# Optimization experiments

Measured on AMD Instinct MI355X. Metric: run time of the kernel, lower is better.

Reference implementation:

```python
import jax, jax.numpy as jnp
import numpy as np

B, T, C, H = 4, 2048, 1024, 16
HS = C // H  # 64
THRESH_INIT = (5 + 1) / 12 * 0.01  # (layer_idx+1)/n_layer * final_token_threshold


def _layernorm(x, w, b, eps=1e-5):
    mu = jnp.mean(x, axis=-1, keepdims=True)
    var = jnp.var(x, axis=-1, keepdims=True)
    return (x - mu) * jax.lax.rsqrt(var + eps) * w + b


def setup_inputs() -> dict:
    key = jax.random.key(0)
    ks = jax.random.split(key, 8)
    s = 0.02
    inp = {
        'x': jax.random.normal(ks[0], (B, T, C), dtype=jnp.float32),
        'attention_mask': jnp.ones((B, T), dtype=jnp.float32),
        'protected_mask': jnp.zeros((B, T), dtype=jnp.float32),
        'ln1_w': jnp.ones((C,), jnp.float32),
        'ln1_b': jnp.zeros((C,), jnp.float32),
        'c_attn_w': jax.random.normal(ks[1], (3 * C, C), jnp.float32) * s,
        'c_attn_b': jnp.zeros((3 * C,), jnp.float32),
        'c_proj_w': jax.random.normal(ks[2], (C, C), jnp.float32) * s,
        'c_proj_b': jnp.zeros((C,), jnp.float32),
        'ln2_w': jnp.ones((C,), jnp.float32),
        'ln2_b': jnp.zeros((C,), jnp.float32),
        'fc_w': jax.random.normal(ks[3], (4 * C, C), jnp.float32) * s,
        'fc_b': jnp.zeros((4 * C,), jnp.float32),
        'fcproj_w': jax.random.normal(ks[4], (C, 4 * C), jnp.float32) * s,
        'fcproj_b': jnp.zeros((C,), jnp.float32),
        'threshold': jnp.asarray(THRESH_INIT, jnp.float32),
    }
    return inp


def reference(x, attention_mask, protected_mask, ln1_w, ln1_b, c_attn_w, c_attn_b,
              c_proj_w, c_proj_b, ln2_w, ln2_b, fc_w, fc_b, fcproj_w, fcproj_b, threshold):
    b, t, c = x.shape
    # --- attention with importance scores ---
    h = _layernorm(x, ln1_w, ln1_b)
    qkv = h @ c_attn_w.T + c_attn_b                      # (B,T,3C)
    q, k, v = jnp.split(qkv, 3, axis=-1)
    q = q.reshape(b, t, H, HS).transpose(0, 2, 1, 3)     # (B,H,T,hs)
    k = k.reshape(b, t, H, HS).transpose(0, 2, 1, 3)
    v = v.reshape(b, t, H, HS).transpose(0, 2, 1, 3)
    att = jnp.einsum('bhqd,bhkd->bhqk', q, k) / np.sqrt(HS)
    causal = jnp.tril(jnp.ones((t, t), dtype=bool))      # (T,T)
    att = jnp.where(causal[None, None], att, -jnp.inf)
    att = jnp.where(attention_mask[:, None, None, :] != 0, att, -jnp.inf)
    att = jax.nn.softmax(att, axis=-1)                   # (B,H,T,T)
    y = jnp.einsum('bhqk,bhkd->bhqd', att, v)
    y = y.transpose(0, 2, 1, 3).reshape(b, t, c)
    y = y @ c_proj_w.T + c_proj_b
    importance = att.mean(axis=1).mean(axis=1)           # (B,T): mean over heads, then queries
    # --- pruning ---
    x = x + y
    pruning_mask = (importance >= threshold).astype(x.dtype)  # hard mode
    pruning_mask = jnp.where(protected_mask > 0, jnp.ones_like(pruning_mask), pruning_mask)
    combined_mask = attention_mask * pruning_mask
    x = x * combined_mask[..., None]
    # --- MLP ---
    m = _layernorm(x, ln2_w, ln2_b)
    m = jax.nn.gelu(m @ fc_w.T + fc_b, approximate=False)
    x = x + (m @ fcproj_w.T + fcproj_b)
    pruning_loss = jnp.asarray(0.0, x.dtype)  # hard mode / lambda=0
    return (x, combined_mask, pruning_loss)
```

## Files before the change

### kernel.cpp

```cpp
#include <hip/hip_runtime.h>
#include <math.h>

#define B_ 4
#define T_ 2048
#define C_ 1024
#define H_ 16
#define NROWS (B_*T_)

typedef short s8v  __attribute__((ext_vector_type(8)));
typedef float f4v  __attribute__((ext_vector_type(4)));
typedef unsigned short u16v4 __attribute__((ext_vector_type(4)));

#define QSCALE 0.1803368801111f

static __device__ __forceinline__ unsigned short f2bf(float x) {
    unsigned u = __float_as_uint(x);
    unsigned r = u + 0x7fffu + ((u >> 16) & 1u);
    return (unsigned short)(r >> 16);
}

static __device__ __forceinline__ float fexp2(float x) {
    return __builtin_amdgcn_exp2f(x);
}

static __device__ __forceinline__ void gload_lds16(const void* g, void* l) {
    __builtin_amdgcn_global_load_lds(
        (const __attribute__((address_space(1))) void*)g,
        (__attribute__((address_space(3))) void*)l, 16, 0, 0);
}

__global__ __launch_bounds__(256) void prep_kernel(
        const float* __restrict__ x, const float* __restrict__ w,
        const float* __restrict__ b, unsigned short* __restrict__ out,
        const float* __restrict__ wsrc, unsigned short* __restrict__ wdst,
        float* __restrict__ imp, int* __restrict__ nsurv)
{
    int row = blockIdx.x;
    int tid = threadIdx.x;
    int widx = row * 96 + tid;
    if (tid < 96) {
        float4 v = ((const float4*)wsrc)[widx];
        u16v4 o = { f2bf(v.x), f2bf(v.y), f2bf(v.z), f2bf(v.w) };
        *(u16v4*)(wdst + (size_t)widx*4) = o;
    }
    if (row < 32) imp[row*256 + tid] = 0.f;
    if (row == 32 && tid < 8) nsurv[tid] = 0;

    const float4* xr = (const float4*)(x + (size_t)row * C_);
    float4 v = xr[tid];
    float s  = v.x + v.y + v.z + v.w;
    float ss = v.x*v.x + v.y*v.y + v.z*v.z + v.w*v.w;
    #pragma unroll
    for (int off = 32; off > 0; off >>= 1) {
        s  += __shfl_down(s,  off, 64);
        ss += __shfl_down(ss, off, 64);
    }
    __shared__ float rs[4], rss[4];
    __shared__ float smu, srstd;
    int wave = tid >> 6, lane = tid & 63;
    if (lane == 0) { rs[wave] = s; rss[wave] = ss; }
    __syncthreads();
    if (tid == 0) {
        float S  = rs[0]+rs[1]+rs[2]+rs[3];
        float SS = rss[0]+rss[1]+rss[2]+rss[3];
        float mu = S * (1.0f/C_);
        float var = SS * (1.0f/C_) - mu*mu;
        smu = mu; srstd = rsqrtf(var + 1e-5f);
    }
    __syncthreads();
    float mu = smu, rstd = srstd;
    float4 wv = ((const float4*)w)[tid];
    float4 bv = ((const float4*)b)[tid];
    u16v4 o;
    o.x = f2bf((v.x-mu)*rstd*wv.x + bv.x);
    o.y = f2bf((v.y-mu)*rstd*wv.y + bv.y);
    o.z = f2bf((v.z-mu)*rstd*wv.z + bv.z);
    o.w = f2bf((v.w-mu)*rstd*wv.w + bv.w);
    *(u16v4*)(out + (size_t)row * C_ + tid*4) = o;
}

__global__ __launch_bounds__(256) void ln_bf16(const float* __restrict__ x,
        const float* __restrict__ w, const float* __restrict__ b,
        unsigned short* __restrict__ out, const int* __restrict__ flag, int nrows)
{
    if (flag && flag[0] == 0) return;
    int tid = threadIdx.x;
    __shared__ float rs[4], rss[4];
    __shared__ float smu, srstd;
    int wave = tid >> 6, lane = tid & 63;
    for (int row = blockIdx.x; row < nrows; row += gridDim.x) {
        const float4* xr = (const float4*)(x + (size_t)row * C_);
        float4 v = xr[tid];
        float s  = v.x + v.y + v.z + v.w;
        float ss = v.x*v.x + v.y*v.y + v.z*v.z + v.w*v.w;
        #pragma unroll
        for (int off = 32; off > 0; off >>= 1) {
            s  += __shfl_down(s,  off, 64);
            ss += __shfl_down(ss, off, 64);
        }
        if (lane == 0) { rs[wave] = s; rss[wave] = ss; }
        __syncthreads();
        if (tid == 0) {
            float S  = rs[0]+rs[1]+rs[2]+rs[3];
            float SS = rss[0]+rss[1]+rss[2]+rss[3];
            float mu = S * (1.0f/C_);
            float var = SS * (1.0f/C_) - mu*mu;
            smu = mu; srstd = rsqrtf(var + 1e-5f);
        }
        __syncthreads();
        float mu = smu, rstd = srstd;
        float4 wv = ((const float4*)w)[tid];
        float4 bv = ((const float4*)b)[tid];
        u16v4 o;
        o.x = f2bf((v.x-mu)*rstd*wv.x + bv.x);
        o.y = f2bf((v.y-mu)*rstd*wv.y + bv.y);
        o.z = f2bf((v.z-mu)*rstd*wv.z + bv.z);
        o.w = f2bf((v.w-mu)*rstd*wv.w + bv.w);
        *(u16v4*)(out + (size_t)row * C_ + tid*4) = o;
        __syncthreads();
    }
}

__global__ __launch_bounds__(256) void cvt3_bf16(
        const float* __restrict__ cprojw, const float* __restrict__ fcw,
        const float* __restrict__ fcpw,
        unsigned short* __restrict__ wproj, unsigned short* __restrict__ wfc,
        unsigned short* __restrict__ wfcp, const int* __restrict__ flag)
{
    if (flag[0] == 0) return;
    const int total = 9*C_*C_/4;
    const int n1 = C_*C_/4;
    const int n2 = n1 + C_*C_;
    for (int i = blockIdx.x * 256 + threadIdx.x; i < total; i += gridDim.x * 256) {
        const float* src; unsigned short* dst; int j;
        if (i < n1)      { src = cprojw; dst = wproj; j = i; }
        else if (i < n2) { src = fcw;    dst = wfc;   j = i - n1; }
        else             { src = fcpw;   dst = wfcp;  j = i - n2; }
        float4 v = ((const float4*)src)[j];
        u16v4 o = { f2bf(v.x), f2bf(v.y), f2bf(v.z), f2bf(v.w) };
        *(u16v4*)(dst + (size_t)j*4) = o;
    }
}

#define STG(gbase_, ldsarr_, ah_, kt_, bb_) do { \
    gload_lds16(gbase_ + (size_t)((ah_)*128)*1024 + (kt_)*64, \
                &ldsarr_[bb_][(((ah_)*128) + (w<<3))*64]); \
    gload_lds16(gbase_ + (size_t)((ah_)*128 + 64)*1024 + (kt_)*64, \
                &ldsarr_[bb_][(((ah_)*128 + 64) + (w<<3))*64]); \
} while (0)

#define PHASE(ah_, bh_, ...) do { \
    s8v af[4][2], bf[2][2]; \
    _Pragma("unroll") \
    for (int i2 = 0; i2 < 4; i2++) { \
        int arow = ((ah_)*128 + wr*64 + i2*16 + l16)*64; \
        af[i2][0] = *(const s8v*)&As[bb][arow + (((quad)     ^ (l16&7))<<3)]; \
        af[i2][1] = *(const s8v*)&As[bb][arow + (((4 + quad) ^ (l16&7))<<3)]; \
    } \
    _Pragma("unroll") \
    for (int j2 = 0; j2 < 2; j2++) { \
        int brow = ((bh_)*128 + wc*32 + j2*16 + l16)*64; \
        bf[j2][0] = *(const s8v*)&Bs[bb][brow + (((quad)     ^ (l16&7))<<3)]; \
        bf[j2][1] = *(const s8v*)&Bs[bb][brow + (((4 + quad) ^ (l16&7))<<3)]; \
    } \
    __VA_ARGS__; \
    asm volatile("s_barrier" ::: "memory"); \
    asm volatile("s_waitcnt lgkmcnt(0)" ::: "memory"); \
    __builtin_amdgcn_sched_barrier(0); \
    __builtin_amdgcn_s_setprio(1); \
    _Pragma("unroll") \
    for (int i2 = 0; i2 < 4; i2++) \
        _Pragma("unroll") \
        for (int j2 = 0; j2 < 2; j2++) { \
            acc[(ah_)*4+i2][(bh_)*2+j2] = __builtin_amdgcn_mfma_f32_16x16x32_bf16( \
                af[i2][0], bf[j2][0], acc[(ah_)*4+i2][(bh_)*2+j2], 0, 0, 0); \
            acc[(ah_)*4+i2][(bh_)*2+j2] = __builtin_amdgcn_mfma_f32_16x16x32_bf16( \
                af[i2][1], bf[j2][1], acc[(ah_)*4+i2][(bh_)*2+j2], 0, 0, 0); \
        } \
    __builtin_amdgcn_s_setprio(0); \
    __builtin_amdgcn_sched_barrier(0); \
    asm volatile("s_barrier" ::: "memory"); \
} while (0)

__global__ __launch_bounds__(512, 2) void gemm_qk_8ph(
    const unsigned short* __restrict__ A,
    const unsigned short* __restrict__ Bw,
    const float* __restrict__ bias,
    unsigned short* __restrict__ qh, unsigned short* __restrict__ kh)
{
    __shared__ unsigned short As[2][256*64];
    __shared__ unsigned short Bs[2][256*64];

    const int tid  = threadIdx.x;
    const int w    = tid >> 6, lane = tid & 63;
// ... 7 lines not shown
    const int m0  = (vb >> 3) << 8;
    const int n0  = (vb & 7) << 8;

    const unsigned short* gA0 = A  + (size_t)(m0 + rl) * 1024 + kc * 8;
    const unsigned short* gB0 = Bw + (size_t)(n0 + rl) * 1024 + kc * 8;

    STG(gA0, As, 0, 0, 0);
    STG(gB0, Bs, 1, 0, 0);
    STG(gA0, As, 1, 0, 0);
    STG(gB0, Bs, 0, 0, 0);
    STG(gA0, As, 0, 1, 1);
    STG(gB0, Bs, 1, 1, 1);

    f4v acc[8][4];
    #pragma unroll
    for (int i = 0; i < 8; i++)
        #pragma unroll
        for (int j = 0; j < 4; j++) {
            acc[i][j][0] = 0.f; acc[i][j][1] = 0.f;
            acc[i][j][2] = 0.f; acc[i][j][3] = 0.f;
        }

    #pragma unroll 2
    for (int t = 0; t < 16; ++t) {
        const int bb = t & 1, nb = bb ^ 1;
        if (t < 15) asm volatile("s_waitcnt vmcnt(4)" ::: "memory");
        else        asm volatile("s_waitcnt vmcnt(0)" ::: "memory");
        asm volatile("s_barrier" ::: "memory");
        __builtin_amdgcn_sched_barrier(0);
        PHASE(0, 0, if (t < 15) STG(gA0, As, 1, t+1, nb));
        PHASE(0, 1, if (t < 15) STG(gB0, Bs, 0, t+1, nb));
        PHASE(1, 1, if (t < 14) STG(gA0, As, 0, t+2, bb));
        PHASE(1, 0, if (t < 14) STG(gB0, Bs, 1, t+2, bb));
    }

    #pragma unroll
    for (int j = 0; j < 4; j++) {
        int ncol = n0 + ((j >> 1) << 7) + (wc << 5) + ((j & 1) << 4) + l16;
        float bv = bias[ncol];
        int sec = ncol >> 10;
        int hh = (ncol & 1023) >> 6, dd = ncol & 63;
        unsigned short* basep = (sec == 0) ? qh : kh;
        bool qsec = (sec == 0);
        #pragma unroll
        for (int i = 0; i < 8; i++) {
            int mbase = m0 + ((i >> 2) << 7) + (wr << 6) + ((i & 3) << 4) + (quad << 2);
            #pragma unroll
            for (int reg = 0; reg < 4; reg++) {
                int m = mbase + reg;
                float v = acc[i][j][reg] + bv;
                if (qsec) v *= QSCALE;
                int b_ = m >> 11, tt = m & 2047;
                basep[(((size_t)(b_*H_ + hh))*T_ + tt)*64 + dd] = f2bf(v);
            }
        }
    }
}

template<int EPI>
__global__ __launch_bounds__(256) void gemm_bf16(
    const unsigned short* __restrict__ A,
    const unsigned short* __restrict__ Bw,
    const float* __restrict__ bias,
    const float* __restrict__ res,
    float* __restrict__ Cout, unsigned short* __restrict__ Cbf,
    int K, int lda, int ldb, int ldc, int ncoff,
    const float* __restrict__ cmv,
    unsigned short* __restrict__ qh, unsigned short* __restrict__ kh,
    unsigned short* __restrict__ vh, const int* __restrict__ flag,
    int nbx, int nby)
{
    if (flag && flag[0] == 0) return;
    __shared__ unsigned short As[128*64];
    __shared__ unsigned short Bs[128*64];
    int tid = threadIdx.x;
    int w = tid >> 6, lane = tid & 63, quad = lane >> 4, l16 = lane & 15;
    int wr = w >> 1, wc = w & 1;

    int nvb = nbx * nby;
    int vb0 = blockIdx.y * gridDim.x + blockIdx.x;
    int vstride = gridDim.x * gridDim.y;

    for (int vb = vb0; vb < nvb; vb += vstride) {
        int n0 = (vb % nbx) * 128;
        int m0 = (vb / nbx) * 128;

        size_t offA[4], offB[4];
        #pragma unroll
        for (int j = 0; j < 4; j++) {
            int ci = j*256 + tid;
            int mr = ci >> 3, kcs = ci & 7;
            int kc = kcs ^ (mr & 7);
            offA[j] = (size_t)(m0 + mr) * lda + kc*8;
            offB[j] = (size_t)(n0 + mr) * ldb + kc*8;
        }

        f4v acc[4][4];
        #pragma unroll
        for (int i = 0; i < 4; i++)
            #pragma unroll
            for (int j = 0; j < 4; j++) { acc[i][j][0]=0.f; acc[i][j][1]=0.f; acc[i][j][2]=0.f; acc[i][j][3]=0.f; }

        for (int k0 = 0; k0 < K; k0 += 64) {
            __syncthreads();
            #pragma unroll
            for (int j = 0; j < 4; j++) {
                gload_lds16(A  + offA[j] + k0, &As[(j*256 + (w<<6))*8]);
                gload_lds16(Bw + offB[j] + k0, &Bs[(j*256 + (w<<6))*8]);
            }
            __syncthreads();
            #pragma unroll
            for (int c = 0; c < 2; c++) {
                s8v af[4], bf[4];
                int sw = ((c<<2) + quad) ^ (l16 & 7);
                #pragma unroll
                for (int i = 0; i < 4; i++) {
                    int mr = wr*64 + i*16 + l16;
                    af[i] = *(const s8v*)&As[mr*64 + sw*8];
                    int nr = wc*64 + i*16 + l16;
                    bf[i] = *(const s8v*)&Bs[nr*64 + sw*8];
                }
                #pragma unroll
                for (int i = 0; i < 4; i++)
                    #pragma unroll
                    for (int j = 0; j < 4; j++)
                        acc[i][j] = __builtin_amdgcn_mfma_f32_16x16x32_bf16(af[i], bf[j], acc[i][j], 0, 0, 0);
            }
        }

        #pragma unroll
        for (int j = 0; j < 4; j++) {
            int ncol = n0 + wc*64 + j*16 + l16;
            float bv = bias ? bias[ncol] : 0.f;
            int hh = 0, dd = 0;
            bool qsec = false;
            unsigned short* basep = nullptr;
            if (EPI == 3) {
                int ncolg = ncol + ncoff;
                int sec = ncolg >> 10;
                int hn = ncolg & 1023;
                hh = hn >> 6; dd = hn & 63;
                basep = (sec == 0) ? qh : (sec == 1) ? kh : vh;
                qsec = (sec == 0);
            }
            #pragma unroll
            for (int i = 0; i < 4; i++) {
                #pragma unroll
                for (int reg = 0; reg < 4; reg++) {
                    int m = m0 + wr*64 + i*16 + quad*4 + reg;
                    float v = acc[i][j][reg] + bv;
                    if (EPI == 1) {
                        v = 0.5f * v * (1.0f + erff(v * 0.70710678118654752f));
                        Cbf[(size_t)m*ldc + ncol] = f2bf(v);
                    } else if (EPI == 2) {
                        Cout[(size_t)m*ldc + ncol] = v + res[(size_t)m*ldc + ncol];
                    } else if (EPI == 3) {
                        if (qsec) v *= QSCALE;
                        int bb = m >> 11, t = m & 2047;
                        basep[(((size_t)(bb*H_ + hh))*T_ + t)*64 + dd] = f2bf(v);
                    } else if (EPI == 4) {
                        Cout[(size_t)m*ldc + ncol] = (res[(size_t)m*ldc + ncol] + v) * cmv[m];
                    }
                }
            }
        }
    }
}

#define RS_LOADK(K_, it_) do { \
    int k0_ = (it_) * 64; \
    _Pragma("unroll") \
    for (int c_ = 0; c_ < 2; c_++) \
        _Pragma("unroll") \
        for (int nt_ = 0; nt_ < 4; nt_++) \
            K_[c_][nt_] = *(const s8v*)(kp + (size_t)(k0_ + nt_*16 + l16)*64 + c_*32 + quad*8); \
} while (0)

#define RS_COMP(K_, it_) do { \
    int k0_ = (it_) * 64; \
    float mk[4]; \
    _Pragma("unroll") \
    for (int nt_ = 0; nt_ < 4; nt_++) mk[nt_] = msk01[k0_ + nt_*16 + l16]; \
    bool allm = __all(mk[0] != 0.f && mk[1] != 0.f && mk[2] != 0.f && mk[3] != 0.f); \
    _Pragma("unroll") \
    for (int qf = 0; qf < 4; qf++) { \
        f4v acc[4]; \
        _Pragma("unroll") \
        for (int nt_ = 0; nt_ < 4; nt_++) { acc[nt_][0]=0.f; acc[nt_][1]=0.f; acc[nt_][2]=0.f; acc[nt_][3]=0.f; } \
        _Pragma("unroll") \
        for (int c_ = 0; c_ < 2; c_++) \
            _Pragma("unroll") \
            for (int nt_ = 0; nt_ < 4; nt_++) \
                acc[nt_] = __builtin_amdgcn_mfma_f32_16x16x32_bf16(aQ[qf][c_], K_[c_][nt_], acc[nt_], 0, 0, 0); \
        if ((it_) < qt && allm) { \
            _Pragma("unroll") \
            for (int nt_ = 0; nt_ < 4; nt_++) \
                _Pragma("unroll") \
                for (int reg = 0; reg < 4; reg++) \
                    lrow[qf][reg] += fexp2(acc[nt_][reg]); \
        } else if ((it_) < qt) { \
            _Pragma("unroll") \
            for (int nt_ = 0; nt_ < 4; nt_++) \
                _Pragma("unroll") \
                for (int reg = 0; reg < 4; reg++) \
                    lrow[qf][reg] += fexp2(acc[nt_][reg]) * mk[nt_]; \
        } else { \
            _Pragma("unroll") \
            for (int nt_ = 0; nt_ < 4; nt_++) { \
                int kg = k0_ + nt_*16 + l16; \
                _Pragma("unroll") \
                for (int reg = 0; reg < 4; reg++) { \
                    float me = (kg <= q0 + qf*16 + quad*4 + reg) ? mk[nt_] : 0.f; \
                    lrow[qf][reg] += fexp2(acc[nt_][reg]) * me; \
                } \
            } \
        } \
// ... 183 lines not shown
                int qt2 = qtn + 4;
                if (qt2 < 32) {
                    CS_LOADQT(AQa, LVa, qt2);
                    CS_COMPQT(AQb, LVb, qtn);
                    qt = qt2;
                    continue;
                } else {
                    CS_COMPQT(AQb, LVb, qtn);
                    break;
                }
            } else {
                CS_COMPQT(AQa, LVa, qt);
                break;
            }
        }
    }

    #pragma unroll
    for (int nt = 0; nt < 4; nt++) {
        float v = cs[nt] * mk[nt];
        v += __shfl_xor(v, 16);
        v += __shfl_xor(v, 32);
        if (quad == 0) cred[w][nt*16 + l16] = v;
    }
    __syncthreads();
    if (tid < 64)
        atomicAdd(&imp[b*T_ + k0 + tid],
                  cred[0][tid] + cred[1][tid] + cred[2][tid] + cred[3][tid]);
}

__global__ __launch_bounds__(256) void mask_finalize(
    const float* __restrict__ imp, const float* __restrict__ amask,
    const float* __restrict__ prot, const float* __restrict__ thr,
    float* __restrict__ mask_out, float* __restrict__ loss_out,
    int* __restrict__ nsurv)
{
    int i = blockIdx.x * 256 + threadIdx.x;
    float impv = imp[i] * (1.0f / (float)(H_ * T_));
    float pm = (impv >= thr[0]) ? 1.f : 0.f;
    if (prot[i] > 0.f) pm = 1.f;
    float cm = amask[i] * pm;
    mask_out[i] = cm;
    if (i == 0) loss_out[0] = 0.f;
    unsigned long long bal = __ballot(cm != 0.f);
    int cnt = __popcll(bal);
    __shared__ int bs;
    if (threadIdx.x == 0) bs = 0;
    __syncthreads();
    if ((threadIdx.x & 63) == 0 && cnt) atomicAdd(&bs, cnt);
    __syncthreads();
    if (threadIdx.x == 0 && bs) atomicAdd(nsurv, bs);
}

__global__ __launch_bounds__(256) void attn_full(
    const unsigned short* __restrict__ qh, const unsigned short* __restrict__ kh,
    const unsigned short* __restrict__ vh, const float* __restrict__ amask,
    unsigned short* __restrict__ y, const int* __restrict__ flag)
{
    if (flag[0] == 0) return;
    __shared__ unsigned short Ks[64][72];
    __shared__ unsigned short Vt[64][72];
    __shared__ unsigned short Ps[4][16][72];
    __shared__ float mks[64];

    int tid = threadIdx.x;
    int w = tid >> 6, lane = tid & 63, quad = lane >> 4, l16 = lane & 15;
    int nqt = T_ / 64;

    for (int vb = blockIdx.x; vb < B_*H_*nqt; vb += gridDim.x) {
        int qt = vb % nqt;
        int bh = vb / nqt;
        int b = bh >> 4, h = bh & 15;
        int q0 = qt * 64;

        const unsigned short* qp = qh + (size_t)bh * T_ * 64;
        const unsigned short* kp = kh + (size_t)bh * T_ * 64;
        const unsigned short* vp = vh + (size_t)bh * T_ * 64;

        int qrow = q0 + 16*w + l16;
        s8v aQ0 = *(const s8v*)(qp + (size_t)qrow*64 + quad*8);
        s8v aQ1 = *(const s8v*)(qp + (size_t)qrow*64 + 32 + quad*8);

        int qwmax = q0 + 16*w + 15;
        int ntiles = qt + 1;
        int qg = q0 + 16*w + quad*4;

        float lrow[4] = {0.f, 0.f, 0.f, 0.f};
        for (int it = 0; it < ntiles; ++it) {
            int k0 = it * 64;
            __syncthreads();
            for (int cid = tid; cid < 512; cid += 256) {
                int row = cid >> 3, ch = cid & 7;
                *(s8v*)&Ks[row][ch*8] = *(const s8v*)(kp + (size_t)(k0+row)*64 + ch*8);
            }
            if (tid < 64) mks[tid] = amask[b*T_ + k0 + tid];
            __syncthreads();
            if (k0 > qwmax) continue;
            f4v accS[4];
            #pragma unroll
            for (int nt = 0; nt < 4; nt++) { accS[nt][0]=0.f; accS[nt][1]=0.f; accS[nt][2]=0.f; accS[nt][3]=0.f; }
            #pragma unroll
            for (int nt = 0; nt < 4; nt++) {
                s8v b0 = *(const s8v*)&Ks[nt*16 + l16][quad*8];
                s8v b1 = *(const s8v*)&Ks[nt*16 + l16][32 + quad*8];
                accS[nt] = __builtin_amdgcn_mfma_f32_16x16x32_bf16(aQ0, b0, accS[nt], 0, 0, 0);
                accS[nt] = __builtin_amdgcn_mfma_f32_16x16x32_bf16(aQ1, b1, accS[nt], 0, 0, 0);
            }
            #pragma unroll
            for (int nt = 0; nt < 4; nt++) {
                int kg = k0 + nt*16 + l16;
                float mkv = mks[nt*16 + l16];
                #pragma unroll
                for (int reg = 0; reg < 4; reg++) {
                    bool val = (kg <= qg + reg) && (mkv != 0.f);
                    float e = fexp2(accS[nt][reg]);
                    lrow[reg] += val ? e : 0.f;
                }
            }
        }
        float linv[4];
        #pragma unroll
        for (int reg = 0; reg < 4; reg++) {
            float v = lrow[reg];
            v += __shfl_xor(v, 1); v += __shfl_xor(v, 2);
            v += __shfl_xor(v, 4); v += __shfl_xor(v, 8);
            linv[reg] = (v > 0.f) ? 1.0f / v : 0.f;
        }

        f4v accO[4];
        #pragma unroll
        for (int nt = 0; nt < 4; nt++) { accO[nt][0]=0.f; accO[nt][1]=0.f; accO[nt][2]=0.f; accO[nt][3]=0.f; }

        for (int it = 0; it < ntiles; ++it) {
            int k0 = it * 64;
            __syncthreads();
            for (int cid = tid; cid < 512; cid += 256) {
                int row = cid >> 3, ch = cid & 7;
                s8v kv = *(const s8v*)(kp + (size_t)(k0+row)*64 + ch*8);
                *(s8v*)&Ks[row][ch*8] = kv;
                s8v vv = *(const s8v*)(vp + (size_t)(k0+row)*64 + ch*8);
                #pragma unroll
                for (int j = 0; j < 8; j++) Vt[ch*8 + j][row] = (unsigned short)vv[j];
            }
            if (tid < 64) mks[tid] = amask[b*T_ + k0 + tid];
            __syncthreads();
            if (k0 > qwmax) continue;
            f4v accS[4];
            #pragma unroll
            for (int nt = 0; nt < 4; nt++) { accS[nt][0]=0.f; accS[nt][1]=0.f; accS[nt][2]=0.f; accS[nt][3]=0.f; }
            #pragma unroll
            for (int nt = 0; nt < 4; nt++) {
                s8v b0 = *(const s8v*)&Ks[nt*16 + l16][quad*8];
                s8v b1 = *(const s8v*)&Ks[nt*16 + l16][32 + quad*8];
                accS[nt] = __builtin_amdgcn_mfma_f32_16x16x32_bf16(aQ0, b0, accS[nt], 0, 0, 0);
                accS[nt] = __builtin_amdgcn_mfma_f32_16x16x32_bf16(aQ1, b1, accS[nt], 0, 0, 0);
            }
            #pragma unroll
            for (int nt = 0; nt < 4; nt++) {
                int kg = k0 + nt*16 + l16;
                float mkv = mks[nt*16 + l16];
                #pragma unroll
                for (int reg = 0; reg < 4; reg++) {
                    bool val = (kg <= qg + reg) && (mkv != 0.f);
                    float p = val ? fexp2(accS[nt][reg]) * linv[reg] : 0.f;
                    Ps[w][quad*4 + reg][nt*16 + l16] = f2bf(p);
                }
            }
            s8v aP0 = *(const s8v*)&Ps[w][l16][quad*8];
            s8v aP1 = *(const s8v*)&Ps[w][l16][32 + quad*8];
            #pragma unroll
            for (int nt = 0; nt < 4; nt++) {
                s8v bv0 = *(const s8v*)&Vt[nt*16 + l16][quad*8];
                s8v bv1 = *(const s8v*)&Vt[nt*16 + l16][32 + quad*8];
                accO[nt] = __builtin_amdgcn_mfma_f32_16x16x32_bf16(aP0, bv0, accO[nt], 0, 0, 0);
                accO[nt] = __builtin_amdgcn_mfma_f32_16x16x32_bf16(aP1, bv1, accO[nt], 0, 0, 0);
            }
        }
        #pragma unroll
        for (int nt = 0; nt < 4; nt++) {
            #pragma unroll
            for (int reg = 0; reg < 4; reg++) {
                int q = q0 + 16*w + quad*4 + reg;
                y[((size_t)(b*T_ + q))*C_ + h*64 + nt*16 + l16] = f2bf(accO[nt][reg]);
            }
        }
        __syncthreads();
    }
}

__global__ __launch_bounds__(256) void ap_fc(const int* __restrict__ nsurv,
        const float* __restrict__ ln2b, const float* __restrict__ fcw,
        const float* __restrict__ fcb, float* __restrict__ abuf)
{
    if (nsurv[0] != 0) return;
    int j = blockIdx.x * 4 + (threadIdx.x >> 6);
    int lane = threadIdx.x & 63;
    const float4* wr = (const float4*)(fcw + (size_t)j * C_);
    const float4* bb = (const float4*)ln2b;
    float s = 0.f;
    #pragma unroll
    for (int k = 0; k < 4; k++) {
        float4 a = bb[lane + 64*k];
        float4 wv = wr[lane + 64*k];
        s += a.x*wv.x + a.y*wv.y + a.z*wv.z + a.w*wv.w;
    }
    #pragma unroll
    for (int off = 32; off > 0; off >>= 1) s += __shfl_down(s, off, 64);
    if (lane == 0) {
        float v = fcb[j] + s;
        abuf[j] = 0.5f * v * (1.0f + erff(v * 0.70710678118654752f));
    }
}

__global__ __launch_bounds__(256) void ap_fcp(const int* __restrict__ nsurv,
        const float* __restrict__ abuf, const float* __restrict__ fcpw,
        const float* __restrict__ fcpb, float* __restrict__ rowbuf)
{
    if (nsurv[0] != 0) return;
    int c = blockIdx.x * 4 + (threadIdx.x >> 6);
    int lane = threadIdx.x & 63;
    const float4* wr = (const float4*)(fcpw + (size_t)c * (4*C_));
    const float4* ab = (const float4*)abuf;
    float s = 0.f;
    #pragma unroll
    for (int k = 0; k < 16; k++) {
        float4 a = ab[lane + 64*k];
        float4 wv = wr[lane + 64*k];
        s += a.x*wv.x + a.y*wv.y + a.z*wv.z + a.w*wv.w;
    }
    #pragma unroll
    for (int off = 32; off > 0; off >>= 1) s += __shfl_down(s, off, 64);
    if (lane == 0) rowbuf[c] = fcpb[c] + s;
}

__global__ __launch_bounds__(256) void ap_bcast(const int* __restrict__ nsurv,
        const float* __restrict__ rowbuf, float* __restrict__ out_x)
{
    if (nsurv[0] != 0) return;
    float4 v = ((const float4*)rowbuf)[threadIdx.x];
    for (int r = blockIdx.x; r < NROWS; r += gridDim.x)
        ((float4*)(out_x + (size_t)r * C_))[threadIdx.x] = v;
}

extern "C" void kernel_launch(void* const* d_in, const int* in_sizes, int n_in,
                              void* d_out, int out_size, void* d_ws, size_t ws_size,
                              hipStream_t stream) {
    const float* x       = (const float*)d_in[0];
    const float* amask   = (const float*)d_in[1];
    const float* prot    = (const float*)d_in[2];
    const float* ln1w    = (const float*)d_in[3];
    const float* ln1b    = (const float*)d_in[4];
    const float* cattn_w = (const float*)d_in[5];
    const float* cattn_b = (const float*)d_in[6];
    const float* cproj_w = (const float*)d_in[7];
    const float* cproj_b = (const float*)d_in[8];
    const float* ln2w    = (const float*)d_in[9];
    const float* ln2b    = (const float*)d_in[10];
    const float* fcw     = (const float*)d_in[11];
    const float* fcb     = (const float*)d_in[12];
    const float* fcpw    = (const float*)d_in[13];
    const float* fcpb    = (const float*)d_in[14];
    const float* thr     = (const float*)d_in[15];

    unsigned short* wqkv  = (unsigned short*)d_ws;
    unsigned short* wproj = wqkv  + (size_t)3*C_*C_;
    unsigned short* wfc   = wproj + (size_t)C_*C_;
    unsigned short* wfcp  = wfc   + (size_t)4*C_*C_;
    unsigned short* hbuf  = wfcp  + (size_t)4*C_*C_;
    unsigned short* qh    = hbuf  + (size_t)NROWS*C_;
    unsigned short* kh    = qh    + (size_t)NROWS*C_;
    unsigned short* vh    = kh    + (size_t)NROWS*C_;
    unsigned short* cbuf  = qh;
    float* imp    = (float*)(vh + (size_t)NROWS*C_);
    int*   nsurv  = (int*)(imp + NROWS);
    float* abuf   = (float*)(nsurv + 8);
    float* rowbuf = abuf + 4*C_;
    float* linvbuf = rowbuf + C_;

    float* out_x    = (float*)d_out;
    float* out_mask = out_x + (size_t)NROWS*C_;
    float* out_loss = out_mask + NROWS;

    hipLaunchKernelGGL(prep_kernel, dim3(NROWS), dim3(256), 0, stream,
                       x, ln1w, ln1b, hbuf, cattn_w, wqkv, imp, nsurv);
    hipLaunchKernelGGL(gemm_qk_8ph, dim3(256), dim3(512), 0, stream,
                       hbuf, wqkv, cattn_b, qh, kh);
    hipLaunchKernelGGL(attn_rowsum, dim3(64*32), dim3(256), 0, stream,
                       qh, kh, amask, linvbuf);
    hipLaunchKernelGGL(attn_colsum, dim3(64*32), dim3(256), 0, stream,
                       qh, kh, amask, linvbuf, imp);
    hipLaunchKernelGGL(mask_finalize, dim3(NROWS/256), dim3(256), 0, stream,
                       imp, amask, prot, thr, out_mask, out_loss, nsurv);

    hipLaunchKernelGGL(cvt3_bf16, dim3(512), dim3(256), 0, stream,
                       cproj_w, fcw, fcpw, wproj, wfc, wfcp, nsurv);
    hipLaunchKernelGGL((gemm_bf16<3>), dim3(512), dim3(256), 0, stream,
                       hbuf, wqkv + (size_t)2048*C_, cattn_b + 2048, nullptr, nullptr, nullptr,
                       C_, C_, C_, 0, 2048, nullptr, qh, kh, vh, nsurv, 8, 64);
    hipLaunchKernelGGL(attn_full, dim3(512), dim3(256), 0, stream,
                       qh, kh, vh, amask, hbuf, nsurv);
    hipLaunchKernelGGL((gemm_bf16<4>), dim3(512), dim3(256), 0, stream,
                       hbuf, wproj, cproj_b, x, out_x, nullptr,
                       C_, C_, C_, C_, 0, out_mask, nullptr, nullptr, nullptr, nsurv, 8, 64);
    hipLaunchKernelGGL(ln_bf16, dim3(512), dim3(256), 0, stream,
                       out_x, ln2w, ln2b, hbuf, nsurv, NROWS);
    for (int j = 0; j < 2; j++) {
        hipLaunchKernelGGL((gemm_bf16<1>), dim3(512), dim3(256), 0, stream,
                           hbuf, wfc + (size_t)j*2048*C_, fcb + j*2048, nullptr, nullptr, cbuf,
                           C_, C_, C_, 2048, 0, nullptr, nullptr, nullptr, nullptr, nsurv, 16, 64);
        hipLaunchKernelGGL((gemm_bf16<2>), dim3(512), dim3(256), 0, stream,
                           cbuf, wfcp + (size_t)j*2048, (j == 0) ? fcpb : nullptr, out_x, out_x, nullptr,
                           2048, 2048, 4*C_, C_, 0, nullptr, nullptr, nullptr, nullptr, nsurv, 8, 64);
    }

    hipLaunchKernelGGL(ap_fc,    dim3(4*C_/4), dim3(256), 0, stream, nsurv, ln2b, fcw, fcb, abuf);
    hipLaunchKernelGGL(ap_fcp,   dim3(C_/4),   dim3(256), 0, stream, nsurv, abuf, fcpw, fcpb, rowbuf);
    hipLaunchKernelGGL(ap_bcast, dim3(512),    dim3(256), 0, stream, nsurv, rowbuf, out_x);
}
```

Baseline: 306.1 us.

## Merge post-mask launches into one persistent kernel with grid barriers

Replaces the chain of conditional tail launches (weight conversion, V projection, attention, projections, layernorm, MLP GEMMs and the all-pruned shortcut kernels) with a single persistent kernel. Phases are separated by a software grid barrier built on atomic counters. This is meant to remove per-launch overhead and the cost of many early-return launches. The risk is deadlock if not all blocks are co-resident, and the fixed 256-block grid may reduce parallelism in the dense path.

```diff
diff --git a/kernel.cpp b/kernel.cpp
--- a/kernel.cpp
+++ b/kernel.cpp
@@ -27,6 +27,25 @@
     __builtin_amdgcn_global_load_lds(
         (const __attribute__((address_space(1))) void*)g,
         (__attribute__((address_space(3))) void*)l, 16, 0, 0);
+}
+
+static __device__ __forceinline__ void gsync(int* bar, int nblk) {
+    __syncthreads();
+    __threadfence();
+    if (threadIdx.x == 0) {
+        int* cnt = bar;
+        int* gen = bar + 1;
+        int g = __hip_atomic_load(gen, __ATOMIC_ACQUIRE, __HIP_MEMORY_SCOPE_AGENT);
+        int a = __hip_atomic_fetch_add(cnt, 1, __ATOMIC_ACQ_REL, __HIP_MEMORY_SCOPE_AGENT);
+        if (a == nblk - 1) {
+            __hip_atomic_store(cnt, 0, __ATOMIC_RELAXED, __HIP_MEMORY_SCOPE_AGENT);
+            __hip_atomic_fetch_add(gen, 1, __ATOMIC_ACQ_REL, __HIP_MEMORY_SCOPE_AGENT);
+        } else {
+            while (__hip_atomic_load(gen, __ATOMIC_ACQUIRE, __HIP_MEMORY_SCOPE_AGENT) == g)
+                __builtin_amdgcn_s_sleep(2);
+        }
+    }
+    __syncthreads();
 }
 
 __global__ __launch_bounds__(256) void prep_kernel(
@@ -77,69 +96,6 @@
     o.z = f2bf((v.z-mu)*rstd*wv.z + bv.z);
     o.w = f2bf((v.w-mu)*rstd*wv.w + bv.w);
     *(u16v4*)(out + (size_t)row * C_ + tid*4) = o;
-}
-
-__global__ __launch_bounds__(256) void ln_bf16(const float* __restrict__ x,
-        const float* __restrict__ w, const float* __restrict__ b,
-        unsigned short* __restrict__ out, const int* __restrict__ flag, int nrows)
-{
-    if (flag && flag[0] == 0) return;
-    int tid = threadIdx.x;
-    __shared__ float rs[4], rss[4];
-    __shared__ float smu, srstd;
-    int wave = tid >> 6, lane = tid & 63;
-    for (int row = blockIdx.x; row < nrows; row += gridDim.x) {
-        const float4* xr = (const float4*)(x + (size_t)row * C_);
-        float4 v = xr[tid];
-        float s  = v.x + v.y + v.z + v.w;
-        float ss = v.x*v.x + v.y*v.y + v.z*v.z + v.w*v.w;
-        #pragma unroll
-        for (int off = 32; off > 0; off >>= 1) {
-            s  += __shfl_down(s,  off, 64);
-            ss += __shfl_down(ss, off, 64);
-        }
-        if (lane == 0) { rs[wave] = s; rss[wave] = ss; }
-        __syncthreads();
-        if (tid == 0) {
-            float S  = rs[0]+rs[1]+rs[2]+rs[3];
-            float SS = rss[0]+rss[1]+rss[2]+rss[3];
-            float mu = S * (1.0f/C_);
-            float var = SS * (1.0f/C_) - mu*mu;
-            smu = mu; srstd = rsqrtf(var + 1e-5f);
-        }
-        __syncthreads();
-        float mu = smu, rstd = srstd;
-        float4 wv = ((const float4*)w)[tid];
-        float4 bv = ((const float4*)b)[tid];
-        u16v4 o;
-        o.x = f2bf((v.x-mu)*rstd*wv.x + bv.x);
-        o.y = f2bf((v.y-mu)*rstd*wv.y + bv.y);
-        o.z = f2bf((v.z-mu)*rstd*wv.z + bv.z);
-        o.w = f2bf((v.w-mu)*rstd*wv.w + bv.w);
-        *(u16v4*)(out + (size_t)row * C_ + tid*4) = o;
-        __syncthreads();
-    }
-}
-
-__global__ __launch_bounds__(256) void cvt3_bf16(
-        const float* __restrict__ cprojw, const float* __restrict__ fcw,
-        const float* __restrict__ fcpw,
-        unsigned short* __restrict__ wproj, unsigned short* __restrict__ wfc,
-        unsigned short* __restrict__ wfcp, const int* __restrict__ flag)
-{
-    if (flag[0] == 0) return;
-    const int total = 9*C_*C_/4;
-    const int n1 = C_*C_/4;
-    const int n2 = n1 + C_*C_;
-    for (int i = blockIdx.x * 256 + threadIdx.x; i < total; i += gridDim.x * 256) {
-        const float* src; unsigned short* dst; int j;
-        if (i < n1)      { src = cprojw; dst = wproj; j = i; }
-        else if (i < n2) { src = fcw;    dst = wfc;   j = i - n1; }
-        else             { src = fcpw;   dst = wfcp;  j = i - n2; }
-        float4 v = ((const float4*)src)[j];
-        u16v4 o = { f2bf(v.x), f2bf(v.y), f2bf(v.z), f2bf(v.w) };
-        *(u16v4*)(dst + (size_t)j*4) = o;
-    }
 }
 
 #define STG(gbase_, ldsarr_, ah_, kt_, bb_) do { \
@@ -253,116 +209,6 @@
                 if (qsec) v *= QSCALE;
                 int b_ = m >> 11, tt = m & 2047;
                 basep[(((size_t)(b_*H_ + hh))*T_ + tt)*64 + dd] = f2bf(v);
-            }
-        }
-    }
-}
-
-template<int EPI>
-__global__ __launch_bounds__(256) void gemm_bf16(
-    const unsigned short* __restrict__ A,
-    const unsigned short* __restrict__ Bw,
-    const float* __restrict__ bias,
-    const float* __restrict__ res,
-    float* __restrict__ Cout, unsigned short* __restrict__ Cbf,
-    int K, int lda, int ldb, int ldc, int ncoff,
-    const float* __restrict__ cmv,
-    unsigned short* __restrict__ qh, unsigned short* __restrict__ kh,
-    unsigned short* __restrict__ vh, const int* __restrict__ flag,
-    int nbx, int nby)
-{
-    if (flag && flag[0] == 0) return;
-    __shared__ unsigned short As[128*64];
-    __shared__ unsigned short Bs[128*64];
-    int tid = threadIdx.x;
-    int w = tid >> 6, lane = tid & 63, quad = lane >> 4, l16 = lane & 15;
-    int wr = w >> 1, wc = w & 1;
-
-    int nvb = nbx * nby;
-    int vb0 = blockIdx.y * gridDim.x + blockIdx.x;
-    int vstride = gridDim.x * gridDim.y;
-
-    for (int vb = vb0; vb < nvb; vb += vstride) {
-        int n0 = (vb % nbx) * 128;
-        int m0 = (vb / nbx) * 128;
-
-        size_t offA[4], offB[4];
-        #pragma unroll
-        for (int j = 0; j < 4; j++) {
-            int ci = j*256 + tid;
-            int mr = ci >> 3, kcs = ci & 7;
-            int kc = kcs ^ (mr & 7);
-            offA[j] = (size_t)(m0 + mr) * lda + kc*8;
-            offB[j] = (size_t)(n0 + mr) * ldb + kc*8;
-        }
-
-        f4v acc[4][4];
-        #pragma unroll
-        for (int i = 0; i < 4; i++)
-            #pragma unroll
-            for (int j = 0; j < 4; j++) { acc[i][j][0]=0.f; acc[i][j][1]=0.f; acc[i][j][2]=0.f; acc[i][j][3]=0.f; }
-
-        for (int k0 = 0; k0 < K; k0 += 64) {
-            __syncthreads();
-            #pragma unroll
-            for (int j = 0; j < 4; j++) {
-                gload_lds16(A  + offA[j] + k0, &As[(j*256 + (w<<6))*8]);
-                gload_lds16(Bw + offB[j] + k0, &Bs[(j*256 + (w<<6))*8]);
-            }
-            __syncthreads();
-            #pragma unroll
-            for (int c = 0; c < 2; c++) {
-                s8v af[4], bf[4];
-                int sw = ((c<<2) + quad) ^ (l16 & 7);
-                #pragma unroll
-                for (int i = 0; i < 4; i++) {
-                    int mr = wr*64 + i*16 + l16;
-                    af[i] = *(const s8v*)&As[mr*64 + sw*8];
-                    int nr = wc*64 + i*16 + l16;
-                    bf[i] = *(const s8v*)&Bs[nr*64 + sw*8];
-                }
-                #pragma unroll
-                for (int i = 0; i < 4; i++)
-                    #pragma unroll
-                    for (int j = 0; j < 4; j++)
-                        acc[i][j] = __builtin_amdgcn_mfma_f32_16x16x32_bf16(af[i], bf[j], acc[i][j], 0, 0, 0);
-            }
-        }
-
-        #pragma unroll
-        for (int j = 0; j < 4; j++) {
-            int ncol = n0 + wc*64 + j*16 + l16;
-            float bv = bias ? bias[ncol] : 0.f;
-            int hh = 0, dd = 0;
-            bool qsec = false;
-            unsigned short* basep = nullptr;
-            if (EPI == 3) {
-                int ncolg = ncol + ncoff;
-                int sec = ncolg >> 10;
-                int hn = ncolg & 1023;
-                hh = hn >> 6; dd = hn & 63;
-                basep = (sec == 0) ? qh : (sec == 1) ? kh : vh;
-                qsec = (sec == 0);
-            }
-            #pragma unroll
-            for (int i = 0; i < 4; i++) {
-                #pragma unroll
-                for (int reg = 0; reg < 4; reg++) {
-                    int m = m0 + wr*64 + i*16 + quad*4 + reg;
-                    float v = acc[i][j][reg] + bv;
-                    if (EPI == 1) {
-                        v = 0.5f * v * (1.0f + erff(v * 0.70710678118654752f));
-                        Cbf[(size_t)m*ldc + ncol] = f2bf(v);
-                    } else if (EPI == 2) {
-                        Cout[(size_t)m*ldc + ncol] = v + res[(size_t)m*ldc + ncol];
-                    } else if (EPI == 3) {
-                        if (qsec) v *= QSCALE;
-                        int bb = m >> 11, t = m & 2047;
-                        basep[(((size_t)(bb*H_ + hh))*T_ + t)*64 + dd] = f2bf(v);
-                    } else if (EPI == 4) {
-                        Cout[(size_t)m*ldc + ncol] = (res[(size_t)m*ldc + ncol] + v) * cmv[m];
-                    }
-                }
             }
         }
     }
@@ -652,16 +498,145 @@
     if (threadIdx.x == 0 && bs) atomicAdd(nsurv, bs);
 }
 
-__global__ __launch_bounds__(256) void attn_full(
+
+static __device__ void cvt3_body(
+        const float* __restrict__ cprojw, const float* __restrict__ fcw,
+        const float* __restrict__ fcpw,
+        unsigned short* __restrict__ wproj, unsigned short* __restrict__ wfc,
+        unsigned short* __restrict__ wfcp)
+{
+    const int total = 9*C_*C_/4;
+    const int n1 = C_*C_/4;
+    const int n2 = n1 + C_*C_;
+    for (int i = blockIdx.x * 256 + threadIdx.x; i < total; i += gridDim.x * 256) {
+        const float* src; unsigned short* dst; int j;
+        if (i < n1)      { src = cprojw; dst = wproj; j = i; }
+        else if (i < n2) { src = fcw;    dst = wfc;   j = i - n1; }
+        else             { src = fcpw;   dst = wfcp;  j = i - n2; }
+        float4 v = ((const float4*)src)[j];
+        u16v4 o = { f2bf(v.x), f2bf(v.y), f2bf(v.z), f2bf(v.w) };
+        *(u16v4*)(dst + (size_t)j*4) = o;
+    }
+}
+
+template<int EPI>
+static __device__ void gemm_body(
+    unsigned short* As, unsigned short* Bs,
+    const unsigned short* __restrict__ A,
+    const unsigned short* __restrict__ Bw,
+    const float* __restrict__ bias,
+    const float* __restrict__ res,
+    float* __restrict__ Cout, unsigned short* __restrict__ Cbf,
+    int K, int lda, int ldb, int ldc, int ncoff,
+    const float* __restrict__ cmv,
+    unsigned short* __restrict__ qh, unsigned short* __restrict__ kh,
+    unsigned short* __restrict__ vh,
+    int nbx, int nby)
+{
+    int tid = threadIdx.x;
+    int w = tid >> 6, lane = tid & 63, quad = lane >> 4, l16 = lane & 15;
+    int wr = w >> 1, wc = w & 1;
+
+    int nvb = nbx * nby;
+    int vb0 = blockIdx.x;
+    int vstride = gridDim.x;
+
+    for (int vb = vb0; vb < nvb; vb += vstride) {
+        int n0 = (vb % nbx) * 128;
+        int m0 = (vb / nbx) * 128;
+
+        size_t offA[4], offB[4];
+        #pragma unroll
+        for (int j = 0; j < 4; j++) {
+            int ci = j*256 + tid;
+            int mr = ci >> 3, kcs = ci & 7;
+            int kc = kcs ^ (mr & 7);
+            offA[j] = (size_t)(m0 + mr) * lda + kc*8;
+            offB[j] = (size_t)(n0 + mr) * ldb + kc*8;
+        }
+
+        f4v acc[4][4];
+        #pragma unroll
+        for (int i = 0; i < 4; i++)
+            #pragma unroll
+            for (int j = 0; j < 4; j++) { acc[i][j][0]=0.f; acc[i][j][1]=0.f; acc[i][j][2]=0.f; acc[i][j][3]=0.f; }
+
+        for (int k0 = 0; k0 < K; k0 += 64) {
+            __syncthreads();
+            #pragma unroll
+            for (int j = 0; j < 4; j++) {
+                gload_lds16(A  + offA[j] + k0, &As[(j*256 + (w<<6))*8]);
+                gload_lds16(Bw + offB[j] + k0, &Bs[(j*256 + (w<<6))*8]);
+            }
+            __syncthreads();
+            #pragma unroll
+            for (int c = 0; c < 2; c++) {
+                s8v af[4], bf[4];
+                int sw = ((c<<2) + quad) ^ (l16 & 7);
+                #pragma unroll
+                for (int i = 0; i < 4; i++) {
+                    int mr = wr*64 + i*16 + l16;
+                    af[i] = *(const s8v*)&As[mr*64 + sw*8];
+                    int nr = wc*64 + i*16 + l16;
+                    bf[i] = *(const s8v*)&Bs[nr*64 + sw*8];
+                }
+                #pragma unroll
+                for (int i = 0; i < 4; i++)
+                    #pragma unroll
+                    for (int j = 0; j < 4; j++)
+                        acc[i][j] = __builtin_amdgcn_mfma_f32_16x16x32_bf16(af[i], bf[j], acc[i][j], 0, 0, 0);
+            }
+        }
+
+        #pragma unroll
+        for (int j = 0; j < 4; j++) {
+            int ncol = n0 + wc*64 + j*16 + l16;
+            float bv = bias ? bias[ncol] : 0.f;
+            int hh = 0, dd = 0;
+            bool qsec = false;
+            unsigned short* basep = nullptr;
+            if (EPI == 3) {
+                int ncolg = ncol + ncoff;
+                int sec = ncolg >> 10;
+                int hn = ncolg & 1023;
+                hh = hn >> 6; dd = hn & 63;
+                basep = (sec == 0) ? qh : (sec == 1) ? kh : vh;
+                qsec = (sec == 0);
+            }
+            #pragma unroll
+            for (int i = 0; i < 4; i++) {
+                #pragma unroll
+                for (int reg = 0; reg < 4; reg++) {
+                    int m = m0 + wr*64 + i*16 + quad*4 + reg;
+                    float v = acc[i][j][reg] + bv;
+                    if (EPI == 1) {
+                        v = 0.5f * v * (1.0f + erff(v * 0.70710678118654752f));
+                        Cbf[(size_t)m*ldc + ncol] = f2bf(v);
+                    } else if (EPI == 2) {
+                        Cout[(size_t)m*ldc + ncol] = v + res[(size_t)m*ldc + ncol];
+                    } else if (EPI == 3) {
+                        if (qsec) v *= QSCALE;
+                        int bb = m >> 11, t = m & 2047;
+                        basep[(((size_t)(bb*H_ + hh))*T_ + t)*64 + dd] = f2bf(v);
+                    } else if (EPI == 4) {
+                        Cout[(size_t)m*ldc + ncol] = (res[(size_t)m*ldc + ncol] + v) * cmv[m];
+                    }
+                }
+            }
+        }
+        __syncthreads();
+    }
+}
+
+static __device__ void attn_full_body(unsigned short* sm,
     const unsigned short* __restrict__ qh, const unsigned short* __restrict__ kh,
     const unsigned short* __restrict__ vh, const float* __restrict__ amask,
-    unsigned short* __restrict__ y, const int* __restrict__ flag)
+    unsigned short* __restrict__ y)
 {
-    if (flag[0] == 0) return;
-    __shared__ unsigned short Ks[64][72];
-    __shared__ unsigned short Vt[64][72];
-    __shared__ unsigned short Ps[4][16][72];
-    __shared__ float mks[64];
+    unsigned short* Ks = sm;
+    unsigned short* Vt = sm + 64*72;
+    unsigned short* Ps = sm + 2*64*72;
+    float* mks = (float*)(sm + 2*64*72 + 4*16*72);
 
     int tid = threadIdx.x;
     int w = tid >> 6, lane = tid & 63, quad = lane >> 4, l16 = lane & 15;
@@ -691,7 +666,7 @@
             __syncthreads();
             for (int cid = tid; cid < 512; cid += 256) {
                 int row = cid >> 3, ch = cid & 7;
-                *(s8v*)&Ks[row][ch*8] = *(const s8v*)(kp + (size_t)(k0+row)*64 + ch*8);
+                *(s8v*)&Ks[row*72 + ch*8] = *(const s8v*)(kp + (size_t)(k0+row)*64 + ch*8);
             }
             if (tid < 64) mks[tid] = amask[b*T_ + k0 + tid];
             __syncthreads();
@@ -701,8 +676,8 @@
             for (int nt = 0; nt < 4; nt++) { accS[nt][0]=0.f; accS[nt][1]=0.f; accS[nt][2]=0.f; accS[nt][3]=0.f; }
             #pragma unroll
             for (int nt = 0; nt < 4; nt++) {
-                s8v b0 = *(const s8v*)&Ks[nt*16 + l16][quad*8];
-                s8v b1 = *(const s8v*)&Ks[nt*16 + l16][32 + quad*8];
+                s8v b0 = *(const s8v*)&Ks[(nt*16 + l16)*72 + quad*8];
+                s8v b1 = *(const s8v*)&Ks[(nt*16 + l16)*72 + 32 + quad*8];
                 accS[nt] = __builtin_amdgcn_mfma_f32_16x16x32_bf16(aQ0, b0, accS[nt], 0, 0, 0);
                 accS[nt] = __builtin_amdgcn_mfma_f32_16x16x32_bf16(aQ1, b1, accS[nt], 0, 0, 0);
             }
@@ -737,10 +712,10 @@
             for (int cid = tid; cid < 512; cid += 256) {
                 int row = cid >> 3, ch = cid & 7;
                 s8v kv = *(const s8v*)(kp + (size_t)(k0+row)*64 + ch*8);
-                *(s8v*)&Ks[row][ch*8] = kv;
+                *(s8v*)&Ks[row*72 + ch*8] = kv;
                 s8v vv = *(const s8v*)(vp + (size_t)(k0+row)*64 + ch*8);
                 #pragma unroll
-                for (int j = 0; j < 8; j++) Vt[ch*8 + j][row] = (unsigned short)vv[j];
+                for (int j = 0; j < 8; j++) Vt[(ch*8 + j)*72 + row] = (unsigned short)vv[j];
             }
             if (tid < 64) mks[tid] = amask[b*T_ + k0 + tid];
             __syncthreads();
@@ -750,8 +725,8 @@
             for (int nt = 0; nt < 4; nt++) { accS[nt][0]=0.f; accS[nt][1]=0.f; accS[nt][2]=0.f; accS[nt][3]=0.f; }
             #pragma unroll
             for (int nt = 0; nt < 4; nt++) {
-                s8v b0 = *(const s8v*)&Ks[nt*16 + l16][quad*8];
-                s8v b1 = *(const s8v*)&Ks[nt*16 + l16][32 + quad*8];
+                s8v b0 = *(const s8v*)&Ks[(nt*16 + l16)*72 + quad*8];
+                s8v b1 = *(const s8v*)&Ks[(nt*16 + l16)*72 + 32 + quad*8];
                 accS[nt] = __builtin_amdgcn_mfma_f32_16x16x32_bf16(aQ0, b0, accS[nt], 0, 0, 0);
                 accS[nt] = __builtin_amdgcn_mfma_f32_16x16x32_bf16(aQ1, b1, accS[nt], 0, 0, 0);
             }
@@ -763,15 +738,15 @@
                 for (int reg = 0; reg < 4; reg++) {
                     bool val = (kg <= qg + reg) && (mkv != 0.f);
                     float p = val ? fexp2(accS[nt][reg]) * linv[reg] : 0.f;
-                    Ps[w][quad*4 + reg][nt*16 + l16] = f2bf(p);
+                    Ps[(w*16 + quad*4 + reg)*72 + nt*16 + l16] = f2bf(p);
                 }
             }
-            s8v aP0 = *(const s8v*)&Ps[w][l16][quad*8];
-            s8v aP1 = *(const s8v*)&Ps[w][l16][32 + quad*8];
+            s8v aP0 = *(const s8v*)&Ps[(w*16 + l16)*72 + quad*8];
+            s8v aP1 = *(const s8v*)&Ps[(w*16 + l16)*72 + 32 + quad*8];
             #pragma unroll
             for (int nt = 0; nt < 4; nt++) {
-                s8v bv0 = *(const s8v*)&Vt[nt*16 + l16][quad*8];
-                s8v bv1 = *(const s8v*)&Vt[nt*16 + l16][32 + quad*8];
+                s8v bv0 = *(const s8v*)&Vt[(nt*16 + l16)*72 + quad*8];
+                s8v bv1 = *(const s8v*)&Vt[(nt*16 + l16)*72 + 32 + quad*8];
                 accO[nt] = __builtin_amdgcn_mfma_f32_16x16x32_bf16(aP0, bv0, accO[nt], 0, 0, 0);
                 accO[nt] = __builtin_amdgcn_mfma_f32_16x16x32_bf16(aP1, bv1, accO[nt], 0, 0, 0);
             }
@@ -788,58 +763,136 @@
     }
 }
 
-__global__ __launch_bounds__(256) void ap_fc(const int* __restrict__ nsurv,
-        const float* __restrict__ ln2b, const float* __restrict__ fcw,
-        const float* __restrict__ fcb, float* __restrict__ abuf)
+static __device__ void ln_body(const float* __restrict__ x,
+        const float* __restrict__ w, const float* __restrict__ b,
+        unsigned short* __restrict__ out, int nrows)
 {
-    if (nsurv[0] != 0) return;
-    int j = blockIdx.x * 4 + (threadIdx.x >> 6);
-    int lane = threadIdx.x & 63;
-    const float4* wr = (const float4*)(fcw + (size_t)j * C_);
-    const float4* bb = (const float4*)ln2b;
-    float s = 0.f;
-    #pragma unroll
-    for (int k = 0; k < 4; k++) {
-        float4 a = bb[lane + 64*k];
-        float4 wv = wr[lane + 64*k];
-        s += a.x*wv.x + a.y*wv.y + a.z*wv.z + a.w*wv.w;
-    }
-    #pragma unroll
-    for (int off = 32; off > 0; off >>= 1) s += __shfl_down(s, off, 64);
-    if (lane == 0) {
-        float v = fcb[j] + s;
-        abuf[j] = 0.5f * v * (1.0f + erff(v * 0.70710678118654752f));
-    }
-}
-
-__global__ __launch_bounds__(256) void ap_fcp(const int* __restrict__ nsurv,
-        const float* __restrict__ abuf, const float* __restrict__ fcpw,
-        const float* __restrict__ fcpb, float* __restrict__ rowbuf)
+    int tid = threadIdx.x;
+    __shared__ float rs[4], rss[4];
+    __shared__ float smu, srstd;
+    int wave = tid >> 6, lane = tid & 63;
+    for (int row = blockIdx.x; row < nrows; row += gridDim.x) {
+        const float4* xr = (const float4*)(x + (size_t)row * C_);
+        float4 v = xr[tid];
+        float s  = v.x + v.y + v.z + v.w;
+        float ss = v.x*v.x + v.y*v.y + v.z*v.z + v.w*v.w;
+        #pragma unroll
+        for (int off = 32; off > 0; off >>= 1) {
+            s  += __shfl_down(s,  off, 64);
+            ss += __shfl_down(ss, off, 64);
+        }
+        if (lane == 0) { rs[wave] = s; rss[wave] = ss; }
+        __syncthreads();
+        if (tid == 0) {
+            float S  = rs[0]+rs[1]+rs[2]+rs[3];
+            float SS = rss[0]+rss[1]+rss[2]+rss[3];
+            float mu = S * (1.0f/C_);
+            float var = SS * (1.0f/C_) - mu*mu;
+            smu = mu; srstd = rsqrtf(var + 1e-5f);
+        }
+        __syncthreads();
+        float mu = smu, rstd = srstd;
+        float4 wv = ((const float4*)w)[tid];
+        float4 bv = ((const float4*)b)[tid];
+        u16v4 o;
+        o.x = f2bf((v.x-mu)*rstd*wv.x + bv.x);
+        o.y = f2bf((v.y-mu)*rstd*wv.y + bv.y);
+        o.z = f2bf((v.z-mu)*rstd*wv.z + bv.z);
+        o.w = f2bf((v.w-mu)*rstd*wv.w + bv.w);
+        *(u16v4*)(out + (size_t)row * C_ + tid*4) = o;
+        __syncthreads();
+    }
+}
+
+__global__ __launch_bounds__(256) void tail_kernel(
+    const float* __restrict__ x, const float* __restrict__ amask,
+    const float* __restrict__ cproj_w, const float* __restrict__ cproj_b,
+    const float* __restrict__ ln2w, const float* __restrict__ ln2b,
+    const float* __restrict__ fcw, const float* __restrict__ fcb,
+    const float* __restrict__ fcpw, const float* __restrict__ fcpb,
+    const float* __restrict__ cattn_b,
+    unsigned short* __restrict__ wqkv, unsigned short* __restrict__ wproj,
+    unsigned short* __restrict__ wfc, unsigned short* __restrict__ wfcp,
+    unsigned short* __restrict__ hbuf,
+    unsigned short* __restrict__ qh, unsigned short* __restrict__ kh,
+    unsigned short* __restrict__ vh, unsigned short* __restrict__ cbuf,
+    float* __restrict__ out_x, float* __restrict__ out_mask,
+    int* __restrict__ nsurv, float* __restrict__ abuf,
+    float* __restrict__ rowbuf)
 {
-    if (nsurv[0] != 0) return;
-    int c = blockIdx.x * 4 + (threadIdx.x >> 6);
-    int lane = threadIdx.x & 63;
-    const float4* wr = (const float4*)(fcpw + (size_t)c * (4*C_));
-    const float4* ab = (const float4*)abuf;
-    float s = 0.f;
-    #pragma unroll
-    for (int k = 0; k < 16; k++) {
-        float4 a = ab[lane + 64*k];
-        float4 wv = wr[lane + 64*k];
-        s += a.x*wv.x + a.y*wv.y + a.z*wv.z + a.w*wv.w;
-    }
-    #pragma unroll
-    for (int off = 32; off > 0; off >>= 1) s += __shfl_down(s, off, 64);
-    if (lane == 0) rowbuf[c] = fcpb[c] + s;
-}
-
-__global__ __launch_bounds__(256) void ap_bcast(const int* __restrict__ nsurv,
-        const float* __restrict__ rowbuf, float* __restrict__ out_x)
-{
-    if (nsurv[0] != 0) return;
-    float4 v = ((const float4*)rowbuf)[threadIdx.x];
+    __shared__ unsigned short smem[2*128*64];
+    unsigned short* As = smem;
+    unsigned short* Bs = smem + 128*64;
+    int* bar = nsurv + 4;
+    const int nblk = gridDim.x;
+
+    const bool dense = (nsurv[0] != 0);
+    int tid = threadIdx.x, w = tid >> 6, lane = tid & 63;
+
+    if (dense) {
+        cvt3_body(cproj_w, fcw, fcpw, wproj, wfc, wfcp);
+        gemm_body<3>(As, Bs, hbuf, wqkv + (size_t)2048*C_, cattn_b + 2048,
+                     nullptr, nullptr, nullptr, C_, C_, C_, 0, 2048, nullptr,
+                     qh, kh, vh, 8, 64);
+        gsync(bar, nblk);
+        attn_full_body(smem, qh, kh, vh, amask, hbuf);
+        gsync(bar, nblk);
+        gemm_body<4>(As, Bs, hbuf, wproj, cproj_b, x, out_x, nullptr,
+                     C_, C_, C_, C_, 0, out_mask, nullptr, nullptr, nullptr, 8, 64);
+        gsync(bar, nblk);
+        ln_body(out_x, ln2w, ln2b, hbuf, NROWS);
+        gsync(bar, nblk);
+        for (int j = 0; j < 2; j++) {
+            gemm_body<1>(As, Bs, hbuf, wfc + (size_t)j*2048*C_, fcb + j*2048,
+                         nullptr, nullptr, cbuf, C_, C_, C_, 2048, 0, nullptr,
+                         nullptr, nullptr, nullptr, 16, 64);
+            gsync(bar, nblk);
+            gemm_body<2>(As, Bs, cbuf, wfcp + (size_t)j*2048, (j == 0) ? fcpb : nullptr,
+                         out_x, out_x, nullptr, 2048, 2048, 4*C_, C_, 0, nullptr,
+                         nullptr, nullptr, nullptr, 8, 64);
+            gsync(bar, nblk);
+        }
+        return;
+    }
+
+    for (int jb = blockIdx.x; jb < C_; jb += gridDim.x) {
+        int j = jb*4 + w;
+        const float4* wr = (const float4*)(fcw + (size_t)j * C_);
+        const float4* bb = (const float4*)ln2b;
+        float s = 0.f;
+        #pragma unroll
+        for (int k = 0; k < 4; k++) {
+            float4 av = bb[lane + 64*k];
+            float4 wv = wr[lane + 64*k];
+            s += av.x*wv.x + av.y*wv.y + av.z*wv.z + av.w*wv.w;
+        }
+        #pragma unroll
+        for (int off = 32; off > 0; off >>= 1) s += __shfl_down(s, off, 64);
+        if (lane == 0) {
+            float v = fcb[j] + s;
+            abuf[j] = 0.5f * v * (1.0f + erff(v * 0.70710678118654752f));
+        }
+    }
+    gsync(bar, nblk);
+    for (int cb = blockIdx.x; cb < C_/4; cb += gridDim.x) {
+        int c = cb*4 + w;
+        const float4* wr = (const float4*)(fcpw + (size_t)c * (4*C_));
+        const float4* ab = (const float4*)abuf;
+        float s = 0.f;
+        #pragma unroll
+        for (int k = 0; k < 16; k++) {
+            float4 av = ab[lane + 64*k];
+            float4 wv = wr[lane + 64*k];
+            s += av.x*wv.x + av.y*wv.y + av.z*wv.z + av.w*wv.w;
+        }
+        #pragma unroll
+        for (int off = 32; off > 0; off >>= 1) s += __shfl_down(s, off, 64);
+        if (lane == 0) rowbuf[c] = fcpb[c] + s;
+    }
+    gsync(bar, nblk);
+    float4 v = ((const float4*)rowbuf)[tid];
     for (int r = blockIdx.x; r < NROWS; r += gridDim.x)
-        ((float4*)(out_x + (size_t)r * C_))[threadIdx.x] = v;
+        ((float4*)(out_x + (size_t)r * C_))[tid] = v;
 }
 
 extern "C" void kernel_launch(void* const* d_in, const int* in_sizes, int n_in,
@@ -892,28 +945,8 @@
     hipLaunchKernelGGL(mask_finalize, dim3(NROWS/256), dim3(256), 0, stream,
                        imp, amask, prot, thr, out_mask, out_loss, nsurv);
 
-    hipLaunchKernelGGL(cvt3_bf16, dim3(512), dim3(256), 0, stream,
-                       cproj_w, fcw, fcpw, wproj, wfc, wfcp, nsurv);
-    hipLaunchKernelGGL((gemm_bf16<3>), dim3(512), dim3(256), 0, stream,
-                       hbuf, wqkv + (size_t)2048*C_, cattn_b + 2048, nullptr, nullptr, nullptr,
-                       C_, C_, C_, 0, 2048, nullptr, qh, kh, vh, nsurv, 8, 64);
-    hipLaunchKernelGGL(attn_full, dim3(512), dim3(256), 0, stream,
-                       qh, kh, vh, amask, hbuf, nsurv);
-    hipLaunchKernelGGL((gemm_bf16<4>), dim3(512), dim3(256), 0, stream,
-                       hbuf, wproj, cproj_b, x, out_x, nullptr,
-                       C_, C_, C_, C_, 0, out_mask, nullptr, nullptr, nullptr, nsurv, 8, 64);
-    hipLaunchKernelGGL(ln_bf16, dim3(512), dim3(256), 0, stream,
-                       out_x, ln2w, ln2b, hbuf, nsurv, NROWS);
-    for (int j = 0; j < 2; j++) {
-        hipLaunchKernelGGL((gemm_bf16<1>), dim3(512), dim3(256), 0, stream,
-                           hbuf, wfc + (size_t)j*2048*C_, fcb + j*2048, nullptr, nullptr, cbuf,
-                           C_, C_, C_, 2048, 0, nullptr, nullptr, nullptr, nullptr, nsurv, 16, 64);
-        hipLaunchKernelGGL((gemm_bf16<2>), dim3(512), dim3(256), 0, stream,
-                           cbuf, wfcp + (size_t)j*2048, (j == 0) ? fcpb : nullptr, out_x, out_x, nullptr,
-                           2048, 2048, 4*C_, C_, 0, nullptr, nullptr, nullptr, nullptr, nsurv, 8, 64);
-    }
-
-    hipLaunchKernelGGL(ap_fc,    dim3(4*C_/4), dim3(256), 0, stream, nsurv, ln2b, fcw, fcb, abuf);
-    hipLaunchKernelGGL(ap_fcp,   dim3(C_/4),   dim3(256), 0, stream, nsurv, abuf, fcpw, fcpb, rowbuf);
-    hipLaunchKernelGGL(ap_bcast, dim3(512),    dim3(256), 0, stream, nsurv, rowbuf, out_x);
-}
+    hipLaunchKernelGGL(tail_kernel, dim3(256), dim3(256), 0, stream,
+                       x, amask, cproj_w, cproj_b, ln2w, ln2b, fcw, fcb,
+                       fcpw, fcpb, cattn_b, wqkv, wproj, wfc, wfcp, hbuf,
+                       qh, kh, vh, cbuf, out_x, out_mask, nsurv, abuf, rowbuf);
+}
```

Result: slower. 372.3 us (+21.6%).
